# Kernel tuning notes

Hardware: AMD Instinct MI355X
Metric: run time of the kernel (lower is better)

Reference implementation:

```python
import jax, jax.numpy as jnp
import numpy as np
from jax import lax


def _conv2d(x, w, b):
    # x: [B,C,H,W], w: [O,I,3,3], 'SAME' padding, stride 1
    y = lax.conv_general_dilated(x, w, (1, 1), 'SAME',
                                 dimension_numbers=('NCHW', 'OIHW', 'NCHW'))
    return y + b[None, :, None, None]


def _grid_sample_border(img, grid):
    # img: [B,C,H,W]; grid: [B,H,W,2] with (x,y) in [-1,1]; align_corners=True,
    # bilinear, padding_mode='border' (coords clamped before interpolation).
    B, C, H, W = img.shape
    ix = jnp.clip((grid[..., 0] + 1.0) * (W - 1) / 2.0, 0.0, W - 1.0)
    iy = jnp.clip((grid[..., 1] + 1.0) * (H - 1) / 2.0, 0.0, H - 1.0)
    x0f = jnp.floor(ix)
    y0f = jnp.floor(iy)
    wx = (ix - x0f)[:, None]  # [B,1,H,W]
    wy = (iy - y0f)[:, None]
    x0 = jnp.clip(x0f.astype(jnp.int32), 0, W - 1)
    x1 = jnp.clip(x0 + 1, 0, W - 1)
    y0 = jnp.clip(y0f.astype(jnp.int32), 0, H - 1)
    y1 = jnp.clip(y0 + 1, 0, H - 1)
    flat = img.reshape(B, C, H * W)

    def gather(yi, xi):
        idx = (yi * W + xi).reshape(B, 1, H * W)
        g = jnp.take_along_axis(flat, jnp.broadcast_to(idx, (B, C, H * W)), axis=2)
        return g.reshape(B, C, H, W)

    v00 = gather(y0, x0)
    v01 = gather(y0, x1)
    v10 = gather(y1, x0)
    v11 = gather(y1, x1)
    top = v00 * (1.0 - wx) + v01 * wx
    bot = v10 * (1.0 - wx) + v11 * wx
    return top * (1.0 - wy) + bot * wy


def setup_inputs() -> dict:
    key = jax.random.key(0)
    ks = jax.random.split(key, 4)
    B, C, H, W = 4, 64, 256, 256
    z_real = jax.random.normal(ks[0], (B, C, H, W), dtype=jnp.float32)
    z_imag = jax.random.normal(ks[1], (B, C, H, W), dtype=jnp.float32)
    fan1 = C * 9
    w1 = jax.random.normal(ks[2], (64, C, 3, 3), dtype=jnp.float32) / np.sqrt(fan1)
    b1 = jnp.zeros((64,), dtype=jnp.float32)
    w2 = jax.random.normal(ks[3], (1, 64, 3, 3), dtype=jnp.float32) / np.sqrt(64 * 9)
    b2 = jnp.zeros((1,), dtype=jnp.float32)
    dt = jnp.float32(0.1)
    return {"z_real": z_real, "z_imag": z_imag, "dt": dt,
            "w1": w1, "b1": b1, "w2": w2, "b2": b2}


def reference(z_real, z_imag, dt, w1, b1, w2, b2):
    B, C, H, W = z_real.shape
    # psi_net: conv -> SiLU -> conv, scaled by dt; psi: [B,1,H,W]
    psi = _conv2d(jax.nn.silu(_conv2d(z_real, w1, b1)), w2, b2) * dt
    # curl with replicate padding, central differences
    p = jnp.pad(psi, ((0, 0), (0, 0), (1, 1), (1, 1)), mode='edge')
    u = (p[:, :, 2:, 1:-1] - p[:, :, :-2, 1:-1]) / 2.0
    v = -(p[:, :, 1:-1, 2:] - p[:, :, 1:-1, :-2]) / 2.0
    # normalized flow: [B,H,W,2]
    flow = jnp.concatenate([u / (W / 2.0), v / (H / 2.0)], axis=1).transpose(0, 2, 3, 1)
    yy, xx = jnp.meshgrid(jnp.linspace(-1.0, 1.0, H), jnp.linspace(-1.0, 1.0, W), indexing='ij')
    base = jnp.stack((xx, yy), axis=-1).astype(z_real.dtype)  # [H,W,2]
    sampling_grid = base[None] - flow
    # sample real and imag in one fused gather over 2C channels
    zc = jnp.concatenate([z_real, z_imag], axis=1)  # [B,2C,H,W]
    out = _grid_sample_border(zc, sampling_grid)
    return out  # [B,2C,H,W]: first C channels = real part, last C = imag part
```

## Files before the change

kernel.cpp:

```cpp
#include <hip/hip_runtime.h>
#include <cmath>

namespace {
constexpr int H = 256, W = 256, HWp = H * W;
constexpr size_t PLANE = (size_t)4 * HWp * 64 * 2;
constexpr size_t NEED_FAST = 73728 + 2 * PLANE + (1u << 20);
}

typedef _Float16 f16;
typedef unsigned int u32;
typedef __attribute__((ext_vector_type(4))) _Float16 f16x4;
typedef __attribute__((ext_vector_type(8))) _Float16 f16x8;
typedef __attribute__((ext_vector_type(4))) float f32x4;
typedef __attribute__((ext_vector_type(4))) unsigned int u32x4;

__device__ __forceinline__ void dma16(const char* g, char* l) {
    __builtin_amdgcn_global_load_lds(
        (const __attribute__((address_space(1))) u32*)g,
        (__attribute__((address_space(3))) u32*)l, 16, 0, 0);
}

__global__ __launch_bounds__(256) void k_xt2(const float* __restrict__ zr,
                                             const float* __restrict__ zi,
                                             f16* __restrict__ Xt_r,
                                             f16* __restrict__ Xt_i,
                                             const float* __restrict__ w1,
                                             f16* __restrict__ w1tb,
                                             int ny_xt) {
    if ((int)blockIdx.y == ny_xt) {
        int i = blockIdx.x * 256 + threadIdx.x;
        if (i < 64 * 576) {
            int co = i / 576, r = i - co * 576;
            int ci = r / 9, k9 = r - ci * 9;
            w1tb[(k9 * 64 + co) * 64 + ci] = (f16)w1[i];
        }
        return;
    }
    __shared__ f16 tile[64][80];
    const int t = threadIdx.x;
    const int p0 = blockIdx.x * 64;
    const int bb = blockIdx.y & 3;
    const bool im = blockIdx.y >= 4;
    const float* x = im ? zi : zr;
    f16* dst = im ? Xt_i : Xt_r;
    const size_t base = (size_t)bb * 64 * HWp;
#pragma unroll
    for (int r = 0; r < 4; ++r) {
        int q = r * 256 + t;
        int ci = q >> 4, px4 = (q & 15) * 4;
        f32x4 v = *reinterpret_cast<const f32x4*>(x + base + (size_t)ci * HWp + p0 + px4);
#pragma unroll
        for (int j = 0; j < 4; ++j) tile[px4 + j][ci] = (f16)v[j];
    }
    __syncthreads();
    const int px = t >> 2, q = t & 3;
    u32x4* d = reinterpret_cast<u32x4*>(dst + ((size_t)bb * HWp + p0 + px) * 64 + q * 16);
    const u32x4* s = reinterpret_cast<const u32x4*>(&tile[px][q * 16]);
    d[0] = s[0];
    d[1] = s[1];
}

__global__ __launch_bounds__(512, 1) void k_conv1(
        const f16* __restrict__ Xt,
        const f16* __restrict__ w1tb,
        const float* __restrict__ b1,
        f16* __restrict__ act) {
    __shared__ __align__(16) char lds[131072];

    const int tid = threadIdx.x;
    const int lane = tid & 63, wid = tid >> 6;
    const int lr = lane & 15, lg = lane >> 4;
    const int pg = wid & 3, cg = wid >> 2;

    const int bid = blockIdx.x;
    const int swz = (bid & 7) * 32 + (bid >> 3);
    const int b = swz >> 6;
    const int y0 = (swz & 63) * 4;

    const int swzb = (lane ^ ((lane >> 3) & 7)) << 4;
    const size_t img = (size_t)b * 256;

    f16x8 Wreg[9][2][2];
#pragma unroll
    for (int k9 = 0; k9 < 9; ++k9)
#pragma unroll
        for (int n = 0; n < 2; ++n)
#pragma unroll
            for (int c = 0; c < 2; ++c)
                Wreg[k9][n][c] = *reinterpret_cast<const f16x8*>(
                    w1tb + (size_t)(k9 * 64 + cg * 32 + n * 16 + lr) * 64
                         + c * 32 + lg * 8);

    float bias[2][4];
#pragma unroll
    for (int n = 0; n < 2; ++n) {
        f32x4 bv = *reinterpret_cast<const f32x4*>(b1 + cg * 32 + n * 16 + lg * 4);
#pragma unroll
        for (int r = 0; r < 4; ++r) bias[n][r] = bv[r];
    }

    auto stage = [&](int yy) {
        const char* src = (const char*)Xt + ((img + yy) * 256) * 128 + swzb;
        char* dst = lds + (yy & 3) * 32768;
#pragma unroll
        for (int i = 0; i < 4; ++i) {
            const int ch = wid + i * 8;
            dma16(src + ch * 1024, dst + ch * 1024);
        }
    };

    if (y0 > 0) stage(y0 - 1);
    stage(y0);
    stage(y0 + 1);
    __syncthreads();

    const f16x8 zf = (f16x8)(f16)0.f;

    for (int r = 0; r < 4; ++r) {
        const int y = y0 + r;
        const int yn = y + 2;
        if (r < 3 && yn < 256) stage(yn);

        f32x4 acc[4][2];
#pragma unroll
        for (int m = 0; m < 4; ++m)
#pragma unroll
            for (int n = 0; n < 2; ++n) acc[m][n] = (f32x4)0.f;

#pragma unroll
        for (int dyi = 0; dyi < 3; ++dyi) {
            const int yy = y + dyi - 1;
            if ((unsigned)yy >= 256u) continue;
            const char* sb = lds + (yy & 3) * 32768;
#pragma unroll
            for (int kx = 0; kx < 3; ++kx) {
                const int dx = kx - 1;
                const int px1 = pg * 64 + 16 + lr + dx;
                const bool ok0 = (unsigned)(px1 - 16) < 256u;
                const bool ok3 = (unsigned)(px1 + 32) < 256u;
                const int px0 = ok0 ? px1 - 16 : px1 - 16 - dx;
                const int px2 = px1 + 16;
                const int px3 = ok3 ? px1 + 32 : px1 + 32 - dx;
                const int k9 = dyi * 3 + kx;
#pragma unroll
                for (int c = 0; c < 2; ++c) {
                    const int pe = c * 4 + lg;
                    f16x8 A0 = *(const f16x8*)(sb + (px0 << 7) + ((pe ^ (px0 & 7)) << 4));
                    f16x8 A1 = *(const f16x8*)(sb + (px1 << 7) + ((pe ^ (px1 & 7)) << 4));
                    f16x8 A2 = *(const f16x8*)(sb + (px2 << 7) + ((pe ^ (px2 & 7)) << 4));
                    f16x8 A3 = *(const f16x8*)(sb + (px3 << 7) + ((pe ^ (px3 & 7)) << 4));
                    A0 = ok0 ? A0 : zf;
                    A3 = ok3 ? A3 : zf;
                    const f16x8 W0 = Wreg[k9][0][c];
                    const f16x8 W1 = Wreg[k9][1][c];
                    acc[0][0] = __builtin_amdgcn_mfma_f32_16x16x32_f16(W0, A0, acc[0][0], 0, 0, 0);
                    acc[0][1] = __builtin_amdgcn_mfma_f32_16x16x32_f16(W1, A0, acc[0][1], 0, 0, 0);
                    acc[1][0] = __builtin_amdgcn_mfma_f32_16x16x32_f16(W0, A1, acc[1][0], 0, 0, 0);
                    acc[1][1] = __builtin_amdgcn_mfma_f32_16x16x32_f16(W1, A1, acc[1][1], 0, 0, 0);
                    acc[2][0] = __builtin_amdgcn_mfma_f32_16x16x32_f16(W0, A2, acc[2][0], 0, 0, 0);
                    acc[2][1] = __builtin_amdgcn_mfma_f32_16x16x32_f16(W1, A2, acc[2][1], 0, 0, 0);
                    acc[3][0] = __builtin_amdgcn_mfma_f32_16x16x32_f16(W0, A3, acc[3][0], 0, 0, 0);
                    acc[3][1] = __builtin_amdgcn_mfma_f32_16x16x32_f16(W1, A3, acc[3][1], 0, 0, 0);
                }
            }
        }

        const size_t rb = (img + y) * 256;
#pragma unroll
        for (int m = 0; m < 4; ++m) {
            f16* ap = act + (rb + pg * 64 + m * 16 + lr) * 64 + cg * 32 + lg * 4;
#pragma unroll
            for (int n = 0; n < 2; ++n) {
                f16x4 o;
#pragma unroll
                for (int q = 0; q < 4; ++q) {
                    float v = acc[m][n][q] + bias[n][q];
                    v = v / (1.f + __expf(-v));
                    o[q] = (f16)v;
                }
                *reinterpret_cast<f16x4*>(ap + n * 16) = o;
            }
        }
        __syncthreads();
    }
}

__global__ __launch_bounds__(256) void k_conv2(
        const f16* __restrict__ act, const float* __restrict__ w2,
        const float* __restrict__ b2, const float* __restrict__ dtp,
        float* __restrict__ psi) {
    const int tx = threadIdx.x & 31, ty = threadIdx.x >> 5;
    const int px = blockIdx.x * 32 + tx;
    const int py = blockIdx.y * 8 + ty;
    const int b = blockIdx.z;

    float a0 = 0.f, a1 = 0.f, a2 = 0.f, a3 = 0.f;
#pragma unroll
    for (int dy = -1; dy <= 1; ++dy) {
        const int yy = py + dy;
        if ((unsigned)yy >= (unsigned)H) continue;
#pragma unroll
        for (int dx = -1; dx <= 1; ++dx) {
            const int xx = px + dx;
            const int k9 = (dy + 1) * 3 + (dx + 1);
            if ((unsigned)xx < (unsigned)W) {
                const f16x8* ap = reinterpret_cast<const f16x8*>(
                    act + (((size_t)b * H + yy) * W + xx) * 64);
                const float* wp = w2 + k9;
#pragma unroll
                for (int g = 0; g < 8; ++g) {
                    const f16x8 v = ap[g];
                    const int cb = g * 8;
                    a0 = fmaf((float)v[0], wp[(cb + 0) * 9], a0);
                    a1 = fmaf((float)v[1], wp[(cb + 1) * 9], a1);
                    a2 = fmaf((float)v[2], wp[(cb + 2) * 9], a2);
                    a3 = fmaf((float)v[3], wp[(cb + 3) * 9], a3);
                    a0 = fmaf((float)v[4], wp[(cb + 4) * 9], a0);
                    a1 = fmaf((float)v[5], wp[(cb + 5) * 9], a1);
                    a2 = fmaf((float)v[6], wp[(cb + 6) * 9], a2);
                    a3 = fmaf((float)v[7], wp[(cb + 7) * 9], a3);
                }
            }
        }
    }
    psi[((size_t)b * H + py) * W + px] = ((a0 + a1) + (a2 + a3) + b2[0]) * dtp[0];
}

__global__ __launch_bounds__(256, 4) void k_sample3(
        const f16* __restrict__ Xt_r, const f16* __restrict__ Xt_i,
        const float* __restrict__ psi, float* __restrict__ out) {
    __shared__ int   s_off[4][128];
    __shared__ float s_w[4][128];
    __shared__ __align__(16) float s_stage[64][132];

    const int tid = threadIdx.x;
    const int bid = blockIdx.x;
    const int swz = (bid & 7) * 256 + (bid >> 3);
    const int seg = swz & 1, y = (swz >> 1) & 255, b = swz >> 9;
    const int x0 = seg * 128;

    if (tid < 128) {
        const int px = x0 + tid;
        const float* pb = psi + b * HWp;
        const int yp = min(y + 1, H - 1), ym = max(y - 1, 0);
        const int xp = min(px + 1, W - 1), xm = max(px - 1, 0);
        const float u = 0.5f * (pb[yp * W + px] - pb[ym * W + px]);
        const float v = -0.5f * (pb[y * W + xp] - pb[y * W + xm]);
        const float gx = (-1.f + 2.f * px / (float)(W - 1)) - u * (2.f / (float)W);
        const float gy = (-1.f + 2.f * y / (float)(H - 1)) - v * (2.f / (float)H);
        float ix = fminf(fmaxf((gx + 1.f) * 0.5f * (float)(W - 1), 0.f), (float)(W - 1));
        float iy = fminf(fmaxf((gy + 1.f) * 0.5f * (float)(H - 1), 0.f), (float)(H - 1));
        const float xf = floorf(ix), yf = floorf(iy);
        const float wx = ix - xf, wy = iy - yf;
        const int ix0 = (int)xf, iy0 = (int)yf;
        const int ix1 = min(ix0 + 1, W - 1), iy1 = min(iy0 + 1, H - 1);
        s_off[0][tid] = (iy0 * W + ix0) * 128;
        s_off[1][tid] = (iy0 * W + ix1) * 128;
        s_off[2][tid] = (iy1 * W + ix0) * 128;
        s_off[3][tid] = (iy1 * W + ix1) * 128;
        s_w[0][tid] = (1.f - wx) * (1.f - wy);
        s_w[1][tid] = wx * (1.f - wy);
        s_w[2][tid] = (1.f - wx) * wy;
        s_w[3][tid] = wx * wy;
    }
    __syncthreads();

    const int p = tid >> 1, s = tid & 1;
    const int o0 = s_off[0][p], o1 = s_off[1][p], o2 = s_off[2][p], o3 = s_off[3][p];
    const float w0 = s_w[0][p], w1 = s_w[1][p], w2 = s_w[2][p], w3 = s_w[3][p];
    const int cl = tid >> 5;
    const int pxq = (tid & 31) * 4;
    const size_t obase = (size_t)b * 128 * HWp + (size_t)y * W + x0 + pxq;

#pragma unroll
    for (int pl = 0; pl < 2; ++pl) {
        const char* base = (const char*)(pl ? Xt_i : Xt_r)
                         + (size_t)b * HWp * 128 + s * 64;
        const char* c0 = base + o0;
        const char* c1 = base + o1;
        const char* c2 = base + o2;
        const char* c3 = base + o3;
        f16x8 h00 = *(const f16x8*)(c0);      f16x8 h01 = *(const f16x8*)(c0 + 16);
        f16x8 h02 = *(const f16x8*)(c0 + 32); f16x8 h03 = *(const f16x8*)(c0 + 48);
        f16x8 h10 = *(const f16x8*)(c1);      f16x8 h11 = *(const f16x8*)(c1 + 16);
        f16x8 h12 = *(const f16x8*)(c1 + 32); f16x8 h13 = *(const f16x8*)(c1 + 48);
        f16x8 h20 = *(const f16x8*)(c2);      f16x8 h21 = *(const f16x8*)(c2 + 16);
        f16x8 h22 = *(const f16x8*)(c2 + 32); f16x8 h23 = *(const f16x8*)(c2 + 48);
        f16x8 h30 = *(const f16x8*)(c3);      f16x8 h31 = *(const f16x8*)(c3 + 16);
        f16x8 h32 = *(const f16x8*)(c3 + 32); f16x8 h33 = *(const f16x8*)(c3 + 48);

        const int rb = s << 5;
#pragma unroll
        for (int k = 0; k < 8; ++k) {
            s_stage[rb + k][p] = w0 * (float)h00[k] + w1 * (float)h10[k]
                               + w2 * (float)h20[k] + w3 * (float)h30[k];
            s_stage[rb + 8 + k][p] = w0 * (float)h01[k] + w1 * (float)h11[k]
                                   + w2 * (float)h21[k] + w3 * (float)h31[k];
            s_stage[rb + 16 + k][p] = w0 * (float)h02[k] + w1 * (float)h12[k]
                                    + w2 * (float)h22[k] + w3 * (float)h32[k];
            s_stage[rb + 24 + k][p] = w0 * (float)h03[k] + w1 * (float)h13[k]
                                    + w2 * (float)h23[k] + w3 * (float)h33[k];
        }
        __syncthreads();
#pragma unroll
        for (int k = 0; k < 8; ++k) {
            const int c = cl + (k << 3);
            f32x4 vv = *(const f32x4*)&s_stage[c][pxq];
            *(f32x4*)(out + obase + (size_t)(pl * 64 + c) * HWp) = vv;
        }
        __syncthreads();
    }
}

__global__ __launch_bounds__(256) void k_sample_fb(
        const float* __restrict__ zr, const float* __restrict__ zi,
        const float* __restrict__ psi, float* __restrict__ out) {
    const int tx = threadIdx.x & 31, ty = threadIdx.x >> 5;
    const int px = blockIdx.x * 32 + tx;
    const int py = blockIdx.y * 8 + ty;
    const int b  = blockIdx.z >> 3;
    const int c0 = (blockIdx.z & 7) * 16;

    const float* pb = psi + b * HWp;
    const int yp = min(py + 1, H - 1), ym = max(py - 1, 0);
    const int xp = min(px + 1, W - 1), xm = max(px - 1, 0);
    const float u = 0.5f * (pb[yp * W + px] - pb[ym * W + px]);
    const float v = -0.5f * (pb[py * W + xp] - pb[py * W + xm]);

    const float gx = (-1.f + 2.f * px / (float)(W - 1)) - u * (2.f / (float)W);
    const float gy = (-1.f + 2.f * py / (float)(H - 1)) - v * (2.f / (float)H);

    float ix = fminf(fmaxf((gx + 1.f) * 0.5f * (float)(W - 1), 0.f), (float)(W - 1));
    float iy = fminf(fmaxf((gy + 1.f) * 0.5f * (float)(H - 1), 0.f), (float)(H - 1));
    const float xf = floorf(ix), yf = floorf(iy);
    const float wx = ix - xf, wy = iy - yf;
    const int ix0 = (int)xf, iy0 = (int)yf;
    const int ix1 = min(ix0 + 1, W - 1), iy1 = min(iy0 + 1, H - 1);

    const int o00 = iy0 * W + ix0, o01 = iy0 * W + ix1;
    const int o10 = iy1 * W + ix0, o11 = iy1 * W + ix1;
    const float w00 = (1.f - wx) * (1.f - wy), w01 = wx * (1.f - wy);
    const float w10 = (1.f - wx) * wy, w11 = wx * wy;

    const float* src0 = (c0 < 64) ? (zr + (size_t)b * 64 * HWp + (size_t)c0 * HWp)
                                  : (zi + (size_t)b * 64 * HWp + (size_t)(c0 - 64) * HWp);
    float* ob = out + ((size_t)b * 128 + c0) * HWp + py * W + px;
#pragma unroll
    for (int c = 0; c < 16; ++c) {
        const float* p = src0 + (size_t)c * HWp;
        ob[(size_t)c * HWp] = p[o00] * w00 + p[o01] * w01 + p[o10] * w10 + p[o11] * w11;
    }
}

extern "C" void kernel_launch(void* const* d_in, const int* in_sizes, int n_in,
                              void* d_out, int out_size, void* d_ws, size_t ws_size,
                              hipStream_t stream) {
    const float* z_real = (const float*)d_in[0];
    const float* z_imag = (const float*)d_in[1];
    const float* dt     = (const float*)d_in[2];
    const float* w1     = (const float*)d_in[3];
    const float* b1     = (const float*)d_in[4];
    const float* w2     = (const float*)d_in[5];
    const float* b2     = (const float*)d_in[6];

    float* out = (float*)d_out;
    char* ws = (char*)d_ws;
    f16* w1tb = (f16*)ws;

    if (ws_size >= NEED_FAST) {
        f16* Xt_r  = (f16*)(ws + 73728);
        f16* Xt_i  = (f16*)(ws + 73728 + PLANE);
        float* psi = (float*)(ws + 73728 + 2 * PLANE);
        f16* act   = (f16*)d_out;

        hipLaunchKernelGGL(k_xt2, dim3(HWp / 64, 9), dim3(256), 0, stream,
                           z_real, z_imag, Xt_r, Xt_i, w1, w1tb, 8);
        hipLaunchKernelGGL(k_conv1, dim3(256), dim3(512), 0, stream, Xt_r, w1tb, b1, act);
        hipLaunchKernelGGL(k_conv2, dim3(8, 32, 4), dim3(256), 0, stream, act, w2, b2, dt, psi);
        hipLaunchKernelGGL(k_sample3, dim3(2048), dim3(256), 0, stream,
                           Xt_r, Xt_i, psi, out);
    } else {
        float* psi = (float*)(ws + 73728);
        f16* Xt  = (f16*)((char*)d_out + 4096);
        f16* act = (f16*)((char*)d_out + 4096 + PLANE);

        hipLaunchKernelGGL(k_xt2, dim3(HWp / 64, 5), dim3(256), 0, stream,
                           z_real, z_real, Xt, Xt, w1, w1tb, 4);
        hipLaunchKernelGGL(k_conv1, dim3(256), dim3(512), 0, stream, Xt, w1tb, b1, act);
        hipLaunchKernelGGL(k_conv2, dim3(8, 32, 4), dim3(256), 0, stream, act, w2, b2, dt, psi);
        hipLaunchKernelGGL(k_sample_fb, dim3(8, 32, 32), dim3(256), 0, stream,
                           z_real, z_imag, psi, out);
    }
}
```

Baseline: 159.9 us.

## Fuse second conv into sampling kernel, computing psi halo in shared memory

Removes the separate conv2 kernel and the psi buffer. Each sampling block now computes psi for a 3x130 halo from the conv1 activations and keeps it in shared memory, then derives the curl and samples as before. The aim is to save one launch and the psi round trip through global memory. In exchange, psi values are recomputed (about 3x overhead) and this serial phase runs before the gather, and act moves into the workspace, which raises the workspace requirement.

```diff
diff --git a/kernel.cpp b/kernel.cpp
--- a/kernel.cpp
+++ b/kernel.cpp
@@ -4,7 +4,7 @@
 namespace {
 constexpr int H = 256, W = 256, HWp = H * W;
 constexpr size_t PLANE = (size_t)4 * HWp * 64 * 2;
-constexpr size_t NEED_FAST = 73728 + 2 * PLANE + (1u << 20);
+constexpr size_t NEED_FAST = 73728 + 3 * PLANE;
 }
 
 typedef _Float16 f16;
@@ -61,10 +61,8 @@
 }
 
 __global__ __launch_bounds__(512, 1) void k_conv1(
-        const f16* __restrict__ Xt,
-        const f16* __restrict__ w1tb,
-        const float* __restrict__ b1,
-        f16* __restrict__ act) {
+        const f16* __restrict__ Xt, const f16* __restrict__ w1tb,
+        const float* __restrict__ b1, f16* __restrict__ act) {
     __shared__ __align__(16) char lds[131072];
 
     const int tid = threadIdx.x;
@@ -226,9 +224,12 @@
     psi[((size_t)b * H + py) * W + px] = ((a0 + a1) + (a2 + a3) + b2[0]) * dtp[0];
 }
 
-__global__ __launch_bounds__(256, 4) void k_sample3(
+__global__ __launch_bounds__(256, 4) void k_psam(
+        const f16* __restrict__ act, const float* __restrict__ w2,
+        const float* __restrict__ b2, const float* __restrict__ dtp,
         const f16* __restrict__ Xt_r, const f16* __restrict__ Xt_i,
-        const float* __restrict__ psi, float* __restrict__ out) {
+        float* __restrict__ out) {
+    __shared__ float psi_s[3][132];
     __shared__ int   s_off[4][128];
     __shared__ float s_w[4][128];
     __shared__ __align__(16) float s_stage[64][132];
@@ -239,13 +240,48 @@
     const int seg = swz & 1, y = (swz >> 1) & 255, b = swz >> 9;
     const int x0 = seg * 128;
 
+    const float dtv = dtp[0], b2v = b2[0];
+    for (int e = tid; e < 390; e += 256) {
+        const int ry = e / 130, rx = e - ry * 130;
+        const int yy = min(max(y - 1 + ry, 0), H - 1);
+        const int xx = min(max(x0 - 1 + rx, 0), W - 1);
+        float a0 = 0.f, a1 = 0.f, a2 = 0.f, a3 = 0.f;
+#pragma unroll
+        for (int dy = -1; dy <= 1; ++dy) {
+            const int qy = yy + dy;
+            if ((unsigned)qy >= (unsigned)H) continue;
+#pragma unroll
+            for (int dx = -1; dx <= 1; ++dx) {
+                const int qx = xx + dx;
+                const int k9 = (dy + 1) * 3 + (dx + 1);
+                if ((unsigned)qx < (unsigned)W) {
+                    const f16x8* ap = reinterpret_cast<const f16x8*>(
+                        act + (((size_t)b * H + qy) * W + qx) * 64);
+                    const float* wp = w2 + k9;
+#pragma unroll
+                    for (int g = 0; g < 8; ++g) {
+                        const f16x8 v = ap[g];
+                        const int cb = g * 8;
+                        a0 = fmaf((float)v[0], wp[(cb + 0) * 9], a0);
+                        a1 = fmaf((float)v[1], wp[(cb + 1) * 9], a1);
+                        a2 = fmaf((float)v[2], wp[(cb + 2) * 9], a2);
+                        a3 = fmaf((float)v[3], wp[(cb + 3) * 9], a3);
+                        a0 = fmaf((float)v[4], wp[(cb + 4) * 9], a0);
+                        a1 = fmaf((float)v[5], wp[(cb + 5) * 9], a1);
+                        a2 = fmaf((float)v[6], wp[(cb + 6) * 9], a2);
+                        a3 = fmaf((float)v[7], wp[(cb + 7) * 9], a3);
+                    }
+                }
+            }
+        }
+        psi_s[ry][rx] = ((a0 + a1) + (a2 + a3) + b2v) * dtv;
+    }
+    __syncthreads();
+
     if (tid < 128) {
         const int px = x0 + tid;
-        const float* pb = psi + b * HWp;
-        const int yp = min(y + 1, H - 1), ym = max(y - 1, 0);
-        const int xp = min(px + 1, W - 1), xm = max(px - 1, 0);
-        const float u = 0.5f * (pb[yp * W + px] - pb[ym * W + px]);
-        const float v = -0.5f * (pb[y * W + xp] - pb[y * W + xm]);
+        const float u = 0.5f * (psi_s[2][tid + 1] - psi_s[0][tid + 1]);
+        const float v = -0.5f * (psi_s[1][tid + 2] - psi_s[1][tid]);
         const float gx = (-1.f + 2.f * px / (float)(W - 1)) - u * (2.f / (float)W);
         const float gy = (-1.f + 2.f * y / (float)(H - 1)) - v * (2.f / (float)H);
         float ix = fminf(fmaxf((gx + 1.f) * 0.5f * (float)(W - 1), 0.f), (float)(W - 1));
@@ -267,7 +303,7 @@
 
     const int p = tid >> 1, s = tid & 1;
     const int o0 = s_off[0][p], o1 = s_off[1][p], o2 = s_off[2][p], o3 = s_off[3][p];
-    const float w0 = s_w[0][p], w1 = s_w[1][p], w2 = s_w[2][p], w3 = s_w[3][p];
+    const float w0 = s_w[0][p], w1 = s_w[1][p], w2v = s_w[2][p], w3 = s_w[3][p];
     const int cl = tid >> 5;
     const int pxq = (tid & 31) * 4;
     const size_t obase = (size_t)b * 128 * HWp + (size_t)y * W + x0 + pxq;
@@ -293,13 +329,13 @@
 #pragma unroll
         for (int k = 0; k < 8; ++k) {
             s_stage[rb + k][p] = w0 * (float)h00[k] + w1 * (float)h10[k]
-                               + w2 * (float)h20[k] + w3 * (float)h30[k];
+                               + w2v * (float)h20[k] + w3 * (float)h30[k];
             s_stage[rb + 8 + k][p] = w0 * (float)h01[k] + w1 * (float)h11[k]
-                                   + w2 * (float)h21[k] + w3 * (float)h31[k];
+                                   + w2v * (float)h21[k] + w3 * (float)h31[k];
             s_stage[rb + 16 + k][p] = w0 * (float)h02[k] + w1 * (float)h12[k]
-                                    + w2 * (float)h22[k] + w3 * (float)h32[k];
+                                    + w2v * (float)h22[k] + w3 * (float)h32[k];
             s_stage[rb + 24 + k][p] = w0 * (float)h03[k] + w1 * (float)h13[k]
-                                    + w2 * (float)h23[k] + w3 * (float)h33[k];
+                                    + w2v * (float)h23[k] + w3 * (float)h33[k];
         }
         __syncthreads();
 #pragma unroll
@@ -368,17 +404,15 @@
     f16* w1tb = (f16*)ws;
 
     if (ws_size >= NEED_FAST) {
-        f16* Xt_r  = (f16*)(ws + 73728);
-        f16* Xt_i  = (f16*)(ws + 73728 + PLANE);
-        float* psi = (float*)(ws + 73728 + 2 * PLANE);
-        f16* act   = (f16*)d_out;
+        f16* Xt_r = (f16*)(ws + 73728);
+        f16* Xt_i = (f16*)(ws + 73728 + PLANE);
+        f16* act  = (f16*)(ws + 73728 + 2 * PLANE);
 
         hipLaunchKernelGGL(k_xt2, dim3(HWp / 64, 9), dim3(256), 0, stream,
                            z_real, z_imag, Xt_r, Xt_i, w1, w1tb, 8);
         hipLaunchKernelGGL(k_conv1, dim3(256), dim3(512), 0, stream, Xt_r, w1tb, b1, act);
-        hipLaunchKernelGGL(k_conv2, dim3(8, 32, 4), dim3(256), 0, stream, act, w2, b2, dt, psi);
-        hipLaunchKernelGGL(k_sample3, dim3(2048), dim3(256), 0, stream,
-                           Xt_r, Xt_i, psi, out);
+        hipLaunchKernelGGL(k_psam, dim3(2048), dim3(256), 0, stream,
+                           act, w2, b2, dt, Xt_r, Xt_i, out);
     } else {
         float* psi = (float*)(ws + 73728);
         f16* Xt  = (f16*)((char*)d_out + 4096);
```

New measurement: 219.7 us. 1.37x slower.

## Compute two conv1 output rows per pass to share LDS fragment loads

Applied to the files above, without the earlier changes.

The conv1 main loop now produces two output rows at once with two accumulator sets. Each of four input rows is read from LDS once and fed to both rows' MFMAs, so activation-fragment reads drop from six rows' worth to four per output pair. Staging changes from a rolling per-row prefetch to loading four rows up front, then two more after the first pair with an extra barrier. This gives up the load/compute overlap of the old pipeline and adds register pressure from the doubled accumulators.

```diff
diff --git a/kernel.cpp b/kernel.cpp
--- a/kernel.cpp
+++ b/kernel.cpp
@@ -61,10 +61,8 @@
 }
 
 __global__ __launch_bounds__(512, 1) void k_conv1(
-        const f16* __restrict__ Xt,
-        const f16* __restrict__ w1tb,
-        const float* __restrict__ b1,
-        f16* __restrict__ act) {
+        const f16* __restrict__ Xt, const f16* __restrict__ w1tb,
+        const float* __restrict__ b1, f16* __restrict__ act) {
     __shared__ __align__(16) char lds[131072];
 
     const int tid = threadIdx.x;
@@ -112,24 +110,24 @@
     if (y0 > 0) stage(y0 - 1);
     stage(y0);
     stage(y0 + 1);
+    stage(y0 + 2);
     __syncthreads();
 
     const f16x8 zf = (f16x8)(f16)0.f;
 
-    for (int r = 0; r < 4; ++r) {
-        const int y = y0 + r;
-        const int yn = y + 2;
-        if (r < 3 && yn < 256) stage(yn);
-
-        f32x4 acc[4][2];
+#pragma unroll
+    for (int pr = 0; pr < 2; ++pr) {
+        const int y = y0 + pr * 2;
+
+        f32x4 acc0[4][2], acc1[4][2];
 #pragma unroll
         for (int m = 0; m < 4; ++m)
 #pragma unroll
-            for (int n = 0; n < 2; ++n) acc[m][n] = (f32x4)0.f;
-
-#pragma unroll
-        for (int dyi = 0; dyi < 3; ++dyi) {
-            const int yy = y + dyi - 1;
+            for (int n = 0; n < 2; ++n) { acc0[m][n] = (f32x4)0.f; acc1[m][n] = (f32x4)0.f; }
+
+#pragma unroll
+        for (int pi = 0; pi < 4; ++pi) {
+            const int yy = y - 1 + pi;
             if ((unsigned)yy >= 256u) continue;
             const char* sb = lds + (yy & 3) * 32768;
 #pragma unroll
@@ -141,7 +139,6 @@
                 const int px0 = ok0 ? px1 - 16 : px1 - 16 - dx;
                 const int px2 = px1 + 16;
                 const int px3 = ok3 ? px1 + 32 : px1 + 32 - dx;
-                const int k9 = dyi * 3 + kx;
 #pragma unroll
                 for (int c = 0; c < 2; ++c) {
                     const int pe = c * 4 + lg;
@@ -151,37 +148,62 @@
                     f16x8 A3 = *(const f16x8*)(sb + (px3 << 7) + ((pe ^ (px3 & 7)) << 4));
                     A0 = ok0 ? A0 : zf;
                     A3 = ok3 ? A3 : zf;
-                    const f16x8 W0 = Wreg[k9][0][c];
-                    const f16x8 W1 = Wreg[k9][1][c];
-                    acc[0][0] = __builtin_amdgcn_mfma_f32_16x16x32_f16(W0, A0, acc[0][0], 0, 0, 0);
-                    acc[0][1] = __builtin_amdgcn_mfma_f32_16x16x32_f16(W1, A0, acc[0][1], 0, 0, 0);
-                    acc[1][0] = __builtin_amdgcn_mfma_f32_16x16x32_f16(W0, A1, acc[1][0], 0, 0, 0);
-                    acc[1][1] = __builtin_amdgcn_mfma_f32_16x16x32_f16(W1, A1, acc[1][1], 0, 0, 0);
-                    acc[2][0] = __builtin_amdgcn_mfma_f32_16x16x32_f16(W0, A2, acc[2][0], 0, 0, 0);
-                    acc[2][1] = __builtin_amdgcn_mfma_f32_16x16x32_f16(W1, A2, acc[2][1], 0, 0, 0);
-                    acc[3][0] = __builtin_amdgcn_mfma_f32_16x16x32_f16(W0, A3, acc[3][0], 0, 0, 0);
-                    acc[3][1] = __builtin_amdgcn_mfma_f32_16x16x32_f16(W1, A3, acc[3][1], 0, 0, 0);
+                    if (pi < 3) {
+                        const int k9 = pi * 3 + kx;
+                        const f16x8 W0 = Wreg[k9][0][c];
+                        const f16x8 W1 = Wreg[k9][1][c];
+                        acc0[0][0] = __builtin_amdgcn_mfma_f32_16x16x32_f16(W0, A0, acc0[0][0], 0, 0, 0);
+                        acc0[0][1] = __builtin_amdgcn_mfma_f32_16x16x32_f16(W1, A0, acc0[0][1], 0, 0, 0);
+                        acc0[1][0] = __builtin_amdgcn_mfma_f32_16x16x32_f16(W0, A1, acc0[1][0], 0, 0, 0);
+                        acc0[1][1] = __builtin_amdgcn_mfma_f32_16x16x32_f16(W1, A1, acc0[1][1], 0, 0, 0);
+                        acc0[2][0] = __builtin_amdgcn_mfma_f32_16x16x32_f16(W0, A2, acc0[2][0], 0, 0, 0);
+                        acc0[2][1] = __builtin_amdgcn_mfma_f32_16x16x32_f16(W1, A2, acc0[2][1], 0, 0, 0);
+                        acc0[3][0] = __builtin_amdgcn_mfma_f32_16x16x32_f16(W0, A3, acc0[3][0], 0, 0, 0);
+                        acc0[3][1] = __builtin_amdgcn_mfma_f32_16x16x32_f16(W1, A3, acc0[3][1], 0, 0, 0);
+                    }
+                    if (pi > 0) {
+                        const int k9 = (pi - 1) * 3 + kx;
+                        const f16x8 W0 = Wreg[k9][0][c];
+                        const f16x8 W1 = Wreg[k9][1][c];
+                        acc1[0][0] = __builtin_amdgcn_mfma_f32_16x16x32_f16(W0, A0, acc1[0][0], 0, 0, 0);
+                        acc1[0][1] = __builtin_amdgcn_mfma_f32_16x16x32_f16(W1, A0, acc1[0][1], 0, 0, 0);
+                        acc1[1][0] = __builtin_amdgcn_mfma_f32_16x16x32_f16(W0, A1, acc1[1][0], 0, 0, 0);
+                        acc1[1][1] = __builtin_amdgcn_mfma_f32_16x16x32_f16(W1, A1, acc1[1][1], 0, 0, 0);
+                        acc1[2][0] = __builtin_amdgcn_mfma_f32_16x16x32_f16(W0, A2, acc1[2][0], 0, 0, 0);
+                        acc1[2][1] = __builtin_amdgcn_mfma_f32_16x16x32_f16(W1, A2, acc1[2][1], 0, 0, 0);
+                        acc1[3][0] = __builtin_amdgcn_mfma_f32_16x16x32_f16(W0, A3, acc1[3][0], 0, 0, 0);
+                        acc1[3][1] = __builtin_amdgcn_mfma_f32_16x16x32_f16(W1, A3, acc1[3][1], 0, 0, 0);
+                    }
                 }
             }
         }
 
-        const size_t rb = (img + y) * 256;
-#pragma unroll
-        for (int m = 0; m < 4; ++m) {
-            f16* ap = act + (rb + pg * 64 + m * 16 + lr) * 64 + cg * 32 + lg * 4;
-#pragma unroll
-            for (int n = 0; n < 2; ++n) {
-                f16x4 o;
-#pragma unroll
-                for (int q = 0; q < 4; ++q) {
-                    float v = acc[m][n][q] + bias[n][q];
-                    v = v / (1.f + __expf(-v));
-                    o[q] = (f16)v;
+#pragma unroll
+        for (int rr = 0; rr < 2; ++rr) {
+            const size_t rb = (img + y + rr) * 256;
+#pragma unroll
+            for (int m = 0; m < 4; ++m) {
+                f16* ap = act + (rb + pg * 64 + m * 16 + lr) * 64 + cg * 32 + lg * 4;
+#pragma unroll
+                for (int n = 0; n < 2; ++n) {
+                    const f32x4 a = rr ? acc1[m][n] : acc0[m][n];
+                    f16x4 o;
+#pragma unroll
+                    for (int q = 0; q < 4; ++q) {
+                        float v = a[q] + bias[n][q];
+                        v = v / (1.f + __expf(-v));
+                        o[q] = (f16)v;
+                    }
+                    *reinterpret_cast<f16x4*>(ap + n * 16) = o;
                 }
-                *reinterpret_cast<f16x4*>(ap + n * 16) = o;
             }
         }
         __syncthreads();
+        if (pr == 0) {
+            if (y0 + 3 < 256) stage(y0 + 3);
+            if (y0 + 4 < 256) stage(y0 + 4);
+            __syncthreads();
+        }
     }
 }
 
```

Measured after the change: 174.2 us. +9.0%, slower.

## Split conv1 tiles into half-row blocks for two blocks per CU

Applied to the files above, without the earlier changes.

Conv1 now launches twice as many 256-thread blocks, each covering a 128-pixel half row plus an 8-pixel halo on each side, with a smaller LDS footprint so two blocks can reside per CU. This is meant to improve occupancy and latency hiding on the MFMA-based convolution. In exchange it loads some redundant halo data, and the halo staging reads slightly outside the row at image edges, relying on masking.

```diff
diff --git a/kernel.cpp b/kernel.cpp
--- a/kernel.cpp
+++ b/kernel.cpp
@@ -60,22 +60,21 @@
     d[1] = s[1];
 }
 
-__global__ __launch_bounds__(512, 1) void k_conv1(
-        const f16* __restrict__ Xt,
-        const f16* __restrict__ w1tb,
-        const float* __restrict__ b1,
-        f16* __restrict__ act) {
-    __shared__ __align__(16) char lds[131072];
+__global__ __launch_bounds__(256, 2) void k_conv1(
+        const f16* __restrict__ Xt, const f16* __restrict__ w1tb,
+        const float* __restrict__ b1, f16* __restrict__ act) {
+    __shared__ __align__(16) char lds[73728];
 
     const int tid = threadIdx.x;
     const int lane = tid & 63, wid = tid >> 6;
     const int lr = lane & 15, lg = lane >> 4;
-    const int pg = wid & 3, cg = wid >> 2;
+    const int pg = wid & 1, cg = wid >> 1;
 
     const int bid = blockIdx.x;
-    const int swz = (bid & 7) * 32 + (bid >> 3);
-    const int b = swz >> 6;
-    const int y0 = (swz & 63) * 4;
+    const int swz = (bid & 7) * 64 + (bid >> 3);
+    const int b = swz >> 7;
+    const int y0 = ((swz >> 1) & 63) * 4;
+    const int x0 = (swz & 1) << 7;
 
     const int swzb = (lane ^ ((lane >> 3) & 7)) << 4;
     const size_t img = (size_t)b * 256;
@@ -100,12 +99,13 @@
     }
 
     auto stage = [&](int yy) {
-        const char* src = (const char*)Xt + ((img + yy) * 256) * 128 + swzb;
-        char* dst = lds + (yy & 3) * 32768;
-#pragma unroll
-        for (int i = 0; i < 4; ++i) {
-            const int ch = wid + i * 8;
-            dma16(src + ch * 1024, dst + ch * 1024);
+        const char* src = (const char*)Xt +
+            ((((size_t)b * 256 + yy) * 256 + x0 - 8) * 128) + swzb;
+        char* dst = lds + (yy & 3) * 18432;
+#pragma unroll
+        for (int i = 0; i < 5; ++i) {
+            const int j = wid + i * 4;
+            if (j < 18) dma16(src + j * 1024, dst + j * 1024);
         }
     };
 
@@ -131,24 +131,25 @@
         for (int dyi = 0; dyi < 3; ++dyi) {
             const int yy = y + dyi - 1;
             if ((unsigned)yy >= 256u) continue;
-            const char* sb = lds + (yy & 3) * 32768;
+            const char* sb = lds + (yy & 3) * 18432;
 #pragma unroll
             for (int kx = 0; kx < 3; ++kx) {
                 const int dx = kx - 1;
-                const int px1 = pg * 64 + 16 + lr + dx;
-                const bool ok0 = (unsigned)(px1 - 16) < 256u;
-                const bool ok3 = (unsigned)(px1 + 32) < 256u;
-                const int px0 = ok0 ? px1 - 16 : px1 - 16 - dx;
-                const int px2 = px1 + 16;
-                const int px3 = ok3 ? px1 + 32 : px1 + 32 - dx;
+                const int gx0 = x0 + pg * 64 + lr + dx;
+                const bool ok0 = (unsigned)gx0 < 256u;
+                const bool ok3 = (unsigned)(gx0 + 48) < 256u;
+                const int loc1 = 8 + pg * 64 + 16 + lr + dx;
+                const int loc0 = ok0 ? loc1 - 16 : loc1 - 16 - dx;
+                const int loc2 = loc1 + 16;
+                const int loc3 = ok3 ? loc1 + 32 : loc1 + 32 - dx;
                 const int k9 = dyi * 3 + kx;
 #pragma unroll
                 for (int c = 0; c < 2; ++c) {
                     const int pe = c * 4 + lg;
-                    f16x8 A0 = *(const f16x8*)(sb + (px0 << 7) + ((pe ^ (px0 & 7)) << 4));
-                    f16x8 A1 = *(const f16x8*)(sb + (px1 << 7) + ((pe ^ (px1 & 7)) << 4));
-                    f16x8 A2 = *(const f16x8*)(sb + (px2 << 7) + ((pe ^ (px2 & 7)) << 4));
-                    f16x8 A3 = *(const f16x8*)(sb + (px3 << 7) + ((pe ^ (px3 & 7)) << 4));
+                    f16x8 A0 = *(const f16x8*)(sb + (loc0 << 7) + ((pe ^ (loc0 & 7)) << 4));
+                    f16x8 A1 = *(const f16x8*)(sb + (loc1 << 7) + ((pe ^ (loc1 & 7)) << 4));
+                    f16x8 A2 = *(const f16x8*)(sb + (loc2 << 7) + ((pe ^ (loc2 & 7)) << 4));
+                    f16x8 A3 = *(const f16x8*)(sb + (loc3 << 7) + ((pe ^ (loc3 & 7)) << 4));
                     A0 = ok0 ? A0 : zf;
                     A3 = ok3 ? A3 : zf;
                     const f16x8 W0 = Wreg[k9][0][c];
@@ -168,7 +169,7 @@
         const size_t rb = (img + y) * 256;
 #pragma unroll
         for (int m = 0; m < 4; ++m) {
-            f16* ap = act + (rb + pg * 64 + m * 16 + lr) * 64 + cg * 32 + lg * 4;
+            f16* ap = act + (rb + x0 + pg * 64 + m * 16 + lr) * 64 + cg * 32 + lg * 4;
 #pragma unroll
             for (int n = 0; n < 2; ++n) {
                 f16x4 o;
@@ -375,7 +376,7 @@
 
         hipLaunchKernelGGL(k_xt2, dim3(HWp / 64, 9), dim3(256), 0, stream,
                            z_real, z_imag, Xt_r, Xt_i, w1, w1tb, 8);
-        hipLaunchKernelGGL(k_conv1, dim3(256), dim3(512), 0, stream, Xt_r, w1tb, b1, act);
+        hipLaunchKernelGGL(k_conv1, dim3(512), dim3(256), 0, stream, Xt_r, w1tb, b1, act);
         hipLaunchKernelGGL(k_conv2, dim3(8, 32, 4), dim3(256), 0, stream, act, w2, b2, dt, psi);
         hipLaunchKernelGGL(k_sample3, dim3(2048), dim3(256), 0, stream,
                            Xt_r, Xt_i, psi, out);
@@ -386,7 +387,7 @@
 
         hipLaunchKernelGGL(k_xt2, dim3(HWp / 64, 5), dim3(256), 0, stream,
                            z_real, z_real, Xt, Xt, w1, w1tb, 4);
-        hipLaunchKernelGGL(k_conv1, dim3(256), dim3(512), 0, stream, Xt, w1tb, b1, act);
+        hipLaunchKernelGGL(k_conv1, dim3(512), dim3(256), 0, stream, Xt, w1tb, b1, act);
         hipLaunchKernelGGL(k_conv2, dim3(8, 32, 4), dim3(256), 0, stream, act, w2, b2, dt, psi);
         hipLaunchKernelGGL(k_sample_fb, dim3(8, 32, 32), dim3(256), 0, stream,
                            z_real, z_imag, psi, out);
```

Result: no change. 162.2 us (+1.5%).
